# Kernel optimization log

Hardware: AMD Instinct MI355X
Metric: run time of the kernel (lower is better)

## Reference

```python
import jax, jax.numpy as jnp
import numpy as np

DIM = 16
FDIM = 16
KNN = 10
N = 1_000_000


def setup_inputs() -> dict:
    key = jax.random.key(0)
    k1, k2, k3, k4, k5, k6 = jax.random.split(key, 6)
    xknn = jax.random.normal(k1, (N, DIM, KNN), dtype=jnp.float32)
    x = jax.random.normal(k2, (N, DIM), dtype=jnp.float32)
    # mlpF = Conv1d(dim, F, 1): weight [F, dim] (kernel size 1 squeezed), bias [F]
    s = 1.0 / np.sqrt(DIM)
    Wf = jax.random.normal(k3, (FDIM, DIM), dtype=jnp.float32) * s
    bf = jax.random.normal(k4, (FDIM,), dtype=jnp.float32) * s
    # mlp1 = Conv1d(F, 1, 1): weight [F], bias scalar
    s1 = 1.0 / np.sqrt(FDIM)
    W1 = jax.random.normal(k5, (FDIM,), dtype=jnp.float32) * s1
    b1 = jax.random.normal(k6, (), dtype=jnp.float32) * s1
    return {"xknn": xknn, "x": x, "Wf": Wf, "bf": bf, "W1": W1, "b1": b1}


def reference(xknn, x, Wf, bf, W1, b1):
    n = xknn.shape[0]
    x2 = xknn.reshape(n, DIM, KNN)                       # [N, dim, K]
    # mlpF on neighbors: Conv1d(dim->F, k=1)
    h2 = jnp.einsum('fd,ndk->nfk', Wf, x2) + bf[:, None]  # [N, F, K]
    a2 = jnp.einsum('f,nfk->nk', W1, h2)[:, None, :] + b1  # mlp1 -> [N, 1, K]
    # mlpF + mlp1 on center point
    x1 = x.reshape(n, DIM, 1)
    h1 = jnp.einsum('fd,ndk->nfk', Wf, x1) + bf[:, None]   # [N, F, 1]
    a1 = jnp.einsum('f,nfk->nk', W1, h1) + b1              # [N, 1] (squeeze+unsqueeze)
    # per-slice additive attention logits (the python loop in the original)
    logits = a2 + a1[:, :, None]                           # [N, 1, K]
    # torch Fn.softmax with implicit dim on 3D tensor -> dim=0 (faithful)
    xc = jax.nn.softmax(logits, axis=0)                    # [N, 1, K]
    # values: mlpF(x2) again, then a raw reshape [N,F,K]->[N,K,F] (not transpose)
    x2v = h2.reshape(n, KNN, FDIM)                         # [N, K, F]
    x_attn = jnp.matmul(xc, x2v)                           # [N, 1, F]
    return x_attn.squeeze(), x2v
```

## Files before the change

kernel.cpp:

```cpp
#include <hip/hip_runtime.h>
#include <math.h>


__device__ __forceinline__ void comb(float& m, float& s, float om, float os) {
  float M = fmaxf(m, om);
  if (M == -INFINITY) return;
  s = s * __expf(m - M) + os * __expf(om - M);
  m = M;
}

template <int CTRL>
__device__ __forceinline__ float qb(float v) {
  return __int_as_float(__builtin_amdgcn_update_dpp(
      0, __float_as_int(v), CTRL, 0xf, 0xf, true));
}

__global__ __launch_bounds__(256) void gap_k1(
    const float* __restrict__ xknn, const float* __restrict__ x,
    const float* __restrict__ Wf, const float* __restrict__ bf,
    const float* __restrict__ W1, const float* __restrict__ b1p,
    float* __restrict__ out, float* __restrict__ partials, int n) {
  __shared__ float s_red[4][16][2];

  const int tid = threadIdx.x;
  const int q = tid & 3;
  const int lane = tid & 63;
  const int wave = tid >> 6;

  float wfq[4][16], w1q[4], bfq[4];
#pragma unroll
  for (int fp = 0; fp < 4; ++fp) {
    const float* wr = Wf + (size_t)(4 * q + fp) * 16;
#pragma unroll
    for (int dq = 0; dq < 4; ++dq) {
      float4 v = *(const float4*)(wr + dq * 4);
      wfq[fp][dq * 4 + 0] = v.x;
      wfq[fp][dq * 4 + 1] = v.y;
      wfq[fp][dq * 4 + 2] = v.z;
      wfq[fp][dq * 4 + 3] = v.w;
    }
    w1q[fp] = W1[4 * q + fp];
    bfq[fp] = bf[4 * q + fp];
  }
  const float b1v = b1p[0];

  float rm[4] = {-INFINITY, -INFINITY, -INFINITY, -INFINITY};
  float rs[4] = {0.f, 0.f, 0.f, 0.f};

  float* out0 = out;
  float* out1 = out + (size_t)n * 16;

  const long quad0 = (long)blockIdx.x * 64 + (tid >> 2);
  const long qstride = (long)gridDim.x * 64;

  for (long pt = quad0; pt < n; pt += qstride) {
    const float* rowq = xknn + (size_t)pt * 160 + 40 * q;
    float4 own[10];
#pragma unroll
    for (int j = 0; j < 10; ++j) own[j] = *(const float4*)(rowq + 4 * j);

    float acc[4][10];
#pragma unroll
    for (int fp = 0; fp < 4; ++fp)
#pragma unroll
      for (int k = 0; k < 10; ++k) acc[fp][k] = bfq[fp];

#pragma unroll
    for (int src = 0; src < 4; ++src) {
#pragma unroll
      for (int rr = 0; rr < 40; ++rr) {
        const int r = src * 40 + rr;
        const int j = rr / 4, e = rr % 4;
        const int d = r / 10, k = r - d * 10;
        const float xe = (e == 0) ? own[j].x
                       : (e == 1) ? own[j].y
                       : (e == 2) ? own[j].z
                                  : own[j].w;
        const float xv = (src == 0)   ? qb<0x00>(xe)
                         : (src == 1) ? qb<0x55>(xe)
                         : (src == 2) ? qb<0xAA>(xe)
                                      : qb<0xFF>(xe);
        acc[0][k] = fmaf(wfq[0][d], xv, acc[0][k]);
        acc[1][k] = fmaf(wfq[1][d], xv, acc[1][k]);
        acc[2][k] = fmaf(wfq[2][d], xv, acc[2][k]);
        acc[3][k] = fmaf(wfq[3][d], xv, acc[3][k]);
      }
    }

    float pa[10];
#pragma unroll
    for (int k = 0; k < 10; ++k) {
      float t = w1q[0] * acc[0][k];
      t = fmaf(w1q[1], acc[1][k], t);
      t = fmaf(w1q[2], acc[2][k], t);
      t = fmaf(w1q[3], acc[3][k], t);
      pa[k] = t;
    }
#pragma unroll
    for (int k = 0; k < 10; ++k) pa[k] += __shfl_xor(pa[k], 1);
#pragma unroll
    for (int k = 0; k < 10; ++k) pa[k] += __shfl_xor(pa[k], 2);

    const float* xr = x + (size_t)pt * 16;
    float h1[4];
#pragma unroll
    for (int fp = 0; fp < 4; ++fp) h1[fp] = bfq[fp];
#pragma unroll
    for (int dq = 0; dq < 4; ++dq) {
      float4 v = *(const float4*)(xr + dq * 4);
      float ve[4] = {v.x, v.y, v.z, v.w};
#pragma unroll
      for (int e = 0; e < 4; ++e)
#pragma unroll
        for (int fp = 0; fp < 4; ++fp)
          h1[fp] = fmaf(wfq[fp][dq * 4 + e], ve[e], h1[fp]);
    }
    float a1p = w1q[0] * h1[0];
    a1p = fmaf(w1q[1], h1[1], a1p);
    a1p = fmaf(w1q[2], h1[2], a1p);
    a1p = fmaf(w1q[3], h1[3], a1p);
    a1p += __shfl_xor(a1p, 1);
    a1p += __shfl_xor(a1p, 2);

    const float addc = a1p + 2.0f * b1v;

    float lj[4];
#pragma unroll
    for (int j = 0; j < 4; ++j) {
      const int k = 4 * q + j;
      float v = 0.f;
#pragma unroll
      for (int kk = 0; kk < 10; ++kk) v = (kk == k) ? (pa[kk] + addc) : v;
      lj[j] = v;
      if (k < 10) comb(rm[j], rs[j], v, 1.0f);
    }
    *(float4*)(out0 + (size_t)pt * 16 + 4 * q) =
        make_float4(lj[0], lj[1], lj[2], lj[3]);

    float vals[40];
#pragma unroll
    for (int fp = 0; fp < 4; ++fp)
#pragma unroll
      for (int k = 0; k < 10; ++k) vals[fp * 10 + k] = acc[fp][k];
    float* o1 = out1 + (size_t)pt * 160 + 40 * q;
#pragma unroll
    for (int i = 0; i < 10; ++i)
      *(float4*)(o1 + 4 * i) = make_float4(vals[4 * i + 0], vals[4 * i + 1],
                                           vals[4 * i + 2], vals[4 * i + 3]);
  }

#pragma unroll
  for (int mask = 4; mask < 64; mask <<= 1) {
#pragma unroll
    for (int j = 0; j < 4; ++j) {
      float om = __shfl_xor(rm[j], mask);
      float os = __shfl_xor(rs[j], mask);
      comb(rm[j], rs[j], om, os);
    }
  }
  if (lane < 4) {
#pragma unroll
    for (int j = 0; j < 4; ++j) {
      s_red[wave][lane * 4 + j][0] = rm[j];
      s_red[wave][lane * 4 + j][1] = rs[j];
    }
  }
  __syncthreads();
  if (tid < 10) {
    float m = s_red[0][tid][0], s = s_red[0][tid][1];
    comb(m, s, s_red[1][tid][0], s_red[1][tid][1]);
    comb(m, s, s_red[2][tid][0], s_red[2][tid][1]);
    comb(m, s, s_red[3][tid][0], s_red[3][tid][1]);
    partials[(size_t)blockIdx.x * 20 + tid * 2 + 0] = m;
    partials[(size_t)blockIdx.x * 20 + tid * 2 + 1] = s;
  }
}

__global__ __launch_bounds__(256) void gap_k2(const float* __restrict__ part,
                                              int nb, float* __restrict__ fin) {
  const int k = blockIdx.x;
  const int tid = threadIdx.x;
  float m = -INFINITY, s = 0.f;
  for (int i = tid; i < nb; i += 256)
    comb(m, s, part[(size_t)i * 20 + k * 2], part[(size_t)i * 20 + k * 2 + 1]);
#pragma unroll
  for (int mask = 1; mask < 64; mask <<= 1) {
    float om = __shfl_xor(m, mask, 64);
    float os = __shfl_xor(s, mask, 64);
    comb(m, s, om, os);
  }
  __shared__ float sm[4][2];
  const int wave = tid >> 6, lane = tid & 63;
  if (lane == 0) { sm[wave][0] = m; sm[wave][1] = s; }
  __syncthreads();
  if (tid == 0) {
    for (int w = 1; w < 4; ++w) comb(m, s, sm[w][0], sm[w][1]);
    fin[k * 2 + 0] = m;
    fin[k * 2 + 1] = s;
  }
}

__global__ __launch_bounds__(256) void gap_k3(const float* __restrict__ fin,
                                              float* __restrict__ out, int n) {
  __shared__ float s_fin[20];
  if (threadIdx.x < 20) s_fin[threadIdx.x] = fin[threadIdx.x];
  __syncthreads();
  float mk[10], rsk[10];
#pragma unroll
  for (int k = 0; k < 10; ++k) {
    mk[k] = s_fin[2 * k];
    rsk[k] = 1.0f / s_fin[2 * k + 1];
  }
  float* out0 = out;
  const float* out1 = out + (size_t)n * 16;
  const int q = threadIdx.x & 3;
  const int pl = threadIdx.x >> 2;
  for (long i = (long)blockIdx.x * 64 + pl; i < n; i += (long)gridDim.x * 64) {
    float* lrow = out0 + i * 16;
    float4 la = *(const float4*)(lrow);
    float4 lb = *(const float4*)(lrow + 4);
    float2 lc = *(const float2*)(lrow + 8);
    float l[10] = {la.x, la.y, la.z, la.w, lb.x, lb.y, lb.z, lb.w, lc.x, lc.y};
    float w[10];
#pragma unroll
    for (int k = 0; k < 10; ++k) w[k] = __expf(l[k] - mk[k]) * rsk[k];
    const float* vrow = out1 + i * 160 + q * 4;
    float4 acc = make_float4(0.f, 0.f, 0.f, 0.f);
#pragma unroll
    for (int k = 0; k < 10; ++k) {
      float4 v = *(const float4*)(vrow + k * 16);
      float wk = w[k];
      acc.x = fmaf(wk, v.x, acc.x);
      acc.y = fmaf(wk, v.y, acc.y);
      acc.z = fmaf(wk, v.z, acc.z);
      acc.w = fmaf(wk, v.w, acc.w);
    }
    *(float4*)(lrow + q * 4) = acc;
  }
}

extern "C" void kernel_launch(void* const* d_in, const int* in_sizes, int n_in,
                              void* d_out, int out_size, void* d_ws, size_t ws_size,
                              hipStream_t stream) {
  const float* xknn = (const float*)d_in[0];
  const float* x    = (const float*)d_in[1];
  const float* Wf   = (const float*)d_in[2];
  const float* bf   = (const float*)d_in[3];
  const float* W1   = (const float*)d_in[4];
  const float* b1   = (const float*)d_in[5];
  float* out = (float*)d_out;
  const int n = in_sizes[1] / 16;

  const int G1 = 2048;
  float* partials = (float*)d_ws;
  float* finals = partials + (size_t)G1 * 20;

  gap_k1<<<G1, 256, 0, stream>>>(xknn, x, Wf, bf, W1, b1, out, partials, n);
  gap_k2<<<10, 256, 0, stream>>>(partials, G1, finals);
  gap_k3<<<2048, 256, 0, stream>>>(finals, out, n);
}
```

Baseline: 562.0 us.

## Software-prefetch next row, fold W1 into Wf for logits, halve k1 grid

The main kernel now loads the next point's xknn and x data into registers while computing the current point, so load latency overlaps with compute. Logits are computed from a precomputed combined vector u = W1·Wf and a folded bias constant, instead of reducing the full hidden activations. This lets the logit path run independently of the DPP-broadcast matmul. The grid is halved and launch bounds request 2 blocks per CU. In exchange, the prefetch buffers raise register pressure and there is extra arithmetic for the separate logit dot products.

```diff
diff --git a/kernel.cpp b/kernel.cpp
--- a/kernel.cpp
+++ b/kernel.cpp
@@ -15,7 +15,11 @@
       0, __float_as_int(v), CTRL, 0xf, 0xf, true));
 }
 
-__global__ __launch_bounds__(256) void gap_k1(
+__device__ __forceinline__ float f4e(const float4& v, int e) {
+  return (e == 0) ? v.x : (e == 1) ? v.y : (e == 2) ? v.z : v.w;
+}
+
+__global__ __launch_bounds__(256, 2) void gap_k1(
     const float* __restrict__ xknn, const float* __restrict__ x,
     const float* __restrict__ Wf, const float* __restrict__ bf,
     const float* __restrict__ W1, const float* __restrict__ b1p,
@@ -27,7 +31,8 @@
   const int lane = tid & 63;
   const int wave = tid >> 6;
 
-  float wfq[4][16], w1q[4], bfq[4];
+  float wfq[4][16], bfq[4];
+  float w1q[4];
 #pragma unroll
   for (int fp = 0; fp < 4; ++fp) {
     const float* wr = Wf + (size_t)(4 * q + fp) * 16;
@@ -44,6 +49,36 @@
   }
   const float b1v = b1p[0];
 
+  float ufull[16];
+#pragma unroll
+  for (int d = 0; d < 16; ++d) {
+    float t = w1q[0] * wfq[0][d];
+    t = fmaf(w1q[1], wfq[1][d], t);
+    t = fmaf(w1q[2], wfq[2][d], t);
+    t = fmaf(w1q[3], wfq[3][d], t);
+    ufull[d] = t;
+  }
+#pragma unroll
+  for (int d = 0; d < 16; ++d) ufull[d] += __shfl_xor(ufull[d], 1);
+#pragma unroll
+  for (int d = 0; d < 16; ++d) ufull[d] += __shfl_xor(ufull[d], 2);
+  float u4[4];
+#pragma unroll
+  for (int i = 0; i < 4; ++i) {
+    float v = ufull[i];
+    v = (q == 1) ? ufull[4 + i] : v;
+    v = (q == 2) ? ufull[8 + i] : v;
+    v = (q == 3) ? ufull[12 + i] : v;
+    u4[i] = v;
+  }
+  float sb = w1q[0] * bfq[0];
+  sb = fmaf(w1q[1], bfq[1], sb);
+  sb = fmaf(w1q[2], bfq[2], sb);
+  sb = fmaf(w1q[3], bfq[3], sb);
+  sb += __shfl_xor(sb, 1);
+  sb += __shfl_xor(sb, 2);
+  const float addK = 2.0f * (sb + b1v);
+
   float rm[4] = {-INFINITY, -INFINITY, -INFINITY, -INFINITY};
   float rs[4] = {0.f, 0.f, 0.f, 0.f};
 
@@ -53,29 +88,58 @@
   const long quad0 = (long)blockIdx.x * 64 + (tid >> 2);
   const long qstride = (long)gridDim.x * 64;
 
+  float4 cur[10], xc;
+  {
+    const long p0 = (quad0 < n) ? quad0 : 0;
+    const float* rowq = xknn + (size_t)p0 * 160 + 40 * q;
+#pragma unroll
+    for (int j = 0; j < 10; ++j) cur[j] = *(const float4*)(rowq + 4 * j);
+    xc = *(const float4*)(x + (size_t)p0 * 16 + 4 * q);
+  }
+
   for (long pt = quad0; pt < n; pt += qstride) {
-    const float* rowq = xknn + (size_t)pt * 160 + 40 * q;
-    float4 own[10];
-#pragma unroll
-    for (int j = 0; j < 10; ++j) own[j] = *(const float4*)(rowq + 4 * j);
+    const long ptn = pt + qstride;
+    const long ptl = (ptn < n) ? ptn : pt;
+    float4 nxt[10], xn;
+    {
+      const float* rowq = xknn + (size_t)ptl * 160 + 40 * q;
+#pragma unroll
+      for (int j = 0; j < 10; ++j) nxt[j] = *(const float4*)(rowq + 4 * j);
+      xn = *(const float4*)(x + (size_t)ptl * 16 + 4 * q);
+    }
+
+    float pa[10];
+#pragma unroll
+    for (int k = 0; k < 10; ++k) pa[k] = 0.f;
+#pragma unroll
+    for (int rr = 0; rr < 40; ++rr) {
+      const int dl = rr / 10, k = rr - dl * 10;
+      pa[k] = fmaf(u4[dl], f4e(cur[rr / 4], rr % 4), pa[k]);
+    }
+    float a1u = u4[0] * xc.x;
+    a1u = fmaf(u4[1], xc.y, a1u);
+    a1u = fmaf(u4[2], xc.z, a1u);
+    a1u = fmaf(u4[3], xc.w, a1u);
+#pragma unroll
+    for (int k = 0; k < 10; ++k) pa[k] += __shfl_xor(pa[k], 1);
+#pragma unroll
+    for (int k = 0; k < 10; ++k) pa[k] += __shfl_xor(pa[k], 2);
+    a1u += __shfl_xor(a1u, 1);
+    a1u += __shfl_xor(a1u, 2);
+    const float addc = a1u + addK;
 
     float acc[4][10];
 #pragma unroll
     for (int fp = 0; fp < 4; ++fp)
 #pragma unroll
       for (int k = 0; k < 10; ++k) acc[fp][k] = bfq[fp];
-
 #pragma unroll
     for (int src = 0; src < 4; ++src) {
 #pragma unroll
       for (int rr = 0; rr < 40; ++rr) {
         const int r = src * 40 + rr;
-        const int j = rr / 4, e = rr % 4;
         const int d = r / 10, k = r - d * 10;
-        const float xe = (e == 0) ? own[j].x
-                       : (e == 1) ? own[j].y
-                       : (e == 2) ? own[j].z
-                                  : own[j].w;
+        const float xe = f4e(cur[rr / 4], rr % 4);
         const float xv = (src == 0)   ? qb<0x00>(xe)
                          : (src == 1) ? qb<0x55>(xe)
                          : (src == 2) ? qb<0xAA>(xe)
@@ -87,43 +151,6 @@
       }
     }
 
-    float pa[10];
-#pragma unroll
-    for (int k = 0; k < 10; ++k) {
-      float t = w1q[0] * acc[0][k];
-      t = fmaf(w1q[1], acc[1][k], t);
-      t = fmaf(w1q[2], acc[2][k], t);
-      t = fmaf(w1q[3], acc[3][k], t);
-      pa[k] = t;
-    }
-#pragma unroll
-    for (int k = 0; k < 10; ++k) pa[k] += __shfl_xor(pa[k], 1);
-#pragma unroll
-    for (int k = 0; k < 10; ++k) pa[k] += __shfl_xor(pa[k], 2);
-
-    const float* xr = x + (size_t)pt * 16;
-    float h1[4];
-#pragma unroll
-    for (int fp = 0; fp < 4; ++fp) h1[fp] = bfq[fp];
-#pragma unroll
-    for (int dq = 0; dq < 4; ++dq) {
-      float4 v = *(const float4*)(xr + dq * 4);
-      float ve[4] = {v.x, v.y, v.z, v.w};
-#pragma unroll
-      for (int e = 0; e < 4; ++e)
-#pragma unroll
-        for (int fp = 0; fp < 4; ++fp)
-          h1[fp] = fmaf(wfq[fp][dq * 4 + e], ve[e], h1[fp]);
-    }
-    float a1p = w1q[0] * h1[0];
-    a1p = fmaf(w1q[1], h1[1], a1p);
-    a1p = fmaf(w1q[2], h1[2], a1p);
-    a1p = fmaf(w1q[3], h1[3], a1p);
-    a1p += __shfl_xor(a1p, 1);
-    a1p += __shfl_xor(a1p, 2);
-
-    const float addc = a1p + 2.0f * b1v;
-
     float lj[4];
 #pragma unroll
     for (int j = 0; j < 4; ++j) {
@@ -137,16 +164,18 @@
     *(float4*)(out0 + (size_t)pt * 16 + 4 * q) =
         make_float4(lj[0], lj[1], lj[2], lj[3]);
 
-    float vals[40];
-#pragma unroll
-    for (int fp = 0; fp < 4; ++fp)
-#pragma unroll
-      for (int k = 0; k < 10; ++k) vals[fp * 10 + k] = acc[fp][k];
     float* o1 = out1 + (size_t)pt * 160 + 40 * q;
 #pragma unroll
-    for (int i = 0; i < 10; ++i)
-      *(float4*)(o1 + 4 * i) = make_float4(vals[4 * i + 0], vals[4 * i + 1],
-                                           vals[4 * i + 2], vals[4 * i + 3]);
+    for (int i = 0; i < 10; ++i) {
+      const int j0 = 4 * i, j1 = 4 * i + 1, j2 = 4 * i + 2, j3 = 4 * i + 3;
+      *(float4*)(o1 + 4 * i) =
+          make_float4(acc[j0 / 10][j0 % 10], acc[j1 / 10][j1 % 10],
+                      acc[j2 / 10][j2 % 10], acc[j3 / 10][j3 % 10]);
+    }
+
+#pragma unroll
+    for (int j = 0; j < 10; ++j) cur[j] = nxt[j];
+    xc = xn;
   }
 
 #pragma unroll
@@ -251,7 +280,7 @@
   float* out = (float*)d_out;
   const int n = in_sizes[1] / 16;
 
-  const int G1 = 2048;
+  const int G1 = 1024;
   float* partials = (float*)d_ws;
   float* finals = partials + (size_t)G1 * 20;
 
```

Result: slower. 1.302 ms (+131.7%).

## Fold mlp1 into mlpF weights for logits, stage Wf in LDS, halve grid

Applied to the files above, without the earlier changes.

Precomputes u = W1·Wf and the folded bias so the attention logits come from a 16-wide dot product on the raw inputs, not a reduction over the 16 features. Wf is staged transposed in shared memory and read as float4 per d instead of being held as 64 registers per thread, which lowers register pressure (launch bounds now request 2 blocks). The k1 grid is halved to 1024 blocks. The change trades per-thread register weights for LDS reads and slightly alters the floating-point summation order.

```diff
diff --git a/kernel.cpp b/kernel.cpp
--- a/kernel.cpp
+++ b/kernel.cpp
@@ -15,11 +15,17 @@
       0, __float_as_int(v), CTRL, 0xf, 0xf, true));
 }
 
-__global__ __launch_bounds__(256) void gap_k1(
+__device__ __forceinline__ float f4e(const float4& v, int e) {
+  return (e == 0) ? v.x : (e == 1) ? v.y : (e == 2) ? v.z : v.w;
+}
+
+__global__ __launch_bounds__(256, 2) void gap_k1(
     const float* __restrict__ xknn, const float* __restrict__ x,
     const float* __restrict__ Wf, const float* __restrict__ bf,
     const float* __restrict__ W1, const float* __restrict__ b1p,
     float* __restrict__ out, float* __restrict__ partials, int n) {
+  __shared__ float s_wfT[16][16];
+  __shared__ float s_w1[16];
   __shared__ float s_red[4][16][2];
 
   const int tid = threadIdx.x;
@@ -27,22 +33,26 @@
   const int lane = tid & 63;
   const int wave = tid >> 6;
 
-  float wfq[4][16], w1q[4], bfq[4];
-#pragma unroll
-  for (int fp = 0; fp < 4; ++fp) {
-    const float* wr = Wf + (size_t)(4 * q + fp) * 16;
-#pragma unroll
-    for (int dq = 0; dq < 4; ++dq) {
-      float4 v = *(const float4*)(wr + dq * 4);
-      wfq[fp][dq * 4 + 0] = v.x;
-      wfq[fp][dq * 4 + 1] = v.y;
-      wfq[fp][dq * 4 + 2] = v.z;
-      wfq[fp][dq * 4 + 3] = v.w;
-    }
-    w1q[fp] = W1[4 * q + fp];
-    bfq[fp] = bf[4 * q + fp];
-  }
-  const float b1v = b1p[0];
+  {
+    const int f = tid & 15, d = tid >> 4;
+    if (tid < 256) s_wfT[d][f] = Wf[f * 16 + d];
+    if (tid < 16) s_w1[tid] = W1[tid];
+  }
+  __syncthreads();
+
+  float u4[4];
+#pragma unroll
+  for (int dd = 0; dd < 4; ++dd) {
+    float t = 0.f;
+#pragma unroll
+    for (int f = 0; f < 16; ++f) t = fmaf(s_w1[f], s_wfT[4 * q + dd][f], t);
+    u4[dd] = t;
+  }
+  float sb = 0.f;
+#pragma unroll
+  for (int f = 0; f < 16; ++f) sb = fmaf(s_w1[f], bf[f], sb);
+  const float addA = sb + 2.0f * b1p[0];
+  const float4 bfq = *(const float4*)(bf + 4 * q);
 
   float rm[4] = {-INFINITY, -INFINITY, -INFINITY, -INFINITY};
   float rs[4] = {0.f, 0.f, 0.f, 0.f};
@@ -50,79 +60,62 @@
   float* out0 = out;
   float* out1 = out + (size_t)n * 16;
 
-  const long quad0 = (long)blockIdx.x * 64 + (tid >> 2);
-  const long qstride = (long)gridDim.x * 64;
-
-  for (long pt = quad0; pt < n; pt += qstride) {
+  const long pt0 = (long)blockIdx.x * 64 + (tid >> 2);
+  const long pstride = (long)gridDim.x * 64;
+
+  for (long pt = pt0; pt < n; pt += pstride) {
     const float* rowq = xknn + (size_t)pt * 160 + 40 * q;
     float4 own[10];
 #pragma unroll
     for (int j = 0; j < 10; ++j) own[j] = *(const float4*)(rowq + 4 * j);
-
-    float acc[4][10];
-#pragma unroll
-    for (int fp = 0; fp < 4; ++fp)
-#pragma unroll
-      for (int k = 0; k < 10; ++k) acc[fp][k] = bfq[fp];
-
-#pragma unroll
-    for (int src = 0; src < 4; ++src) {
-#pragma unroll
-      for (int rr = 0; rr < 40; ++rr) {
-        const int r = src * 40 + rr;
-        const int j = rr / 4, e = rr % 4;
-        const int d = r / 10, k = r - d * 10;
-        const float xe = (e == 0) ? own[j].x
-                       : (e == 1) ? own[j].y
-                       : (e == 2) ? own[j].z
-                                  : own[j].w;
-        const float xv = (src == 0)   ? qb<0x00>(xe)
-                         : (src == 1) ? qb<0x55>(xe)
-                         : (src == 2) ? qb<0xAA>(xe)
-                                      : qb<0xFF>(xe);
-        acc[0][k] = fmaf(wfq[0][d], xv, acc[0][k]);
-        acc[1][k] = fmaf(wfq[1][d], xv, acc[1][k]);
-        acc[2][k] = fmaf(wfq[2][d], xv, acc[2][k]);
-        acc[3][k] = fmaf(wfq[3][d], xv, acc[3][k]);
+    const float4 xc4 = *(const float4*)(x + (size_t)pt * 16 + 4 * q);
+
+    float pa[10];
+#pragma unroll
+    for (int k = 0; k < 10; ++k) pa[k] = 0.f;
+#pragma unroll
+    for (int rr = 0; rr < 40; ++rr) {
+      const int dl = rr / 10, k = rr - dl * 10;
+      pa[k] = fmaf(u4[dl], f4e(own[rr >> 2], rr & 3), pa[k]);
+    }
+#pragma unroll
+    for (int k = 0; k < 10; ++k) pa[k] += __shfl_xor(pa[k], 1);
+#pragma unroll
+    for (int k = 0; k < 10; ++k) pa[k] += __shfl_xor(pa[k], 2);
+    float a1u = u4[0] * xc4.x;
+    a1u = fmaf(u4[1], xc4.y, a1u);
+    a1u = fmaf(u4[2], xc4.z, a1u);
+    a1u = fmaf(u4[3], xc4.w, a1u);
+    a1u += __shfl_xor(a1u, 1);
+    a1u += __shfl_xor(a1u, 2);
+    const float addc = a1u + addA;
+
+    float acc0[10], acc1[10], acc2[10], acc3[10];
+#pragma unroll
+    for (int k = 0; k < 10; ++k) {
+      acc0[k] = bfq.x;
+      acc1[k] = bfq.y;
+      acc2[k] = bfq.z;
+      acc3[k] = bfq.w;
+    }
+#pragma unroll
+    for (int d = 0; d < 16; ++d) {
+      const float4 wfv = *(const float4*)(&s_wfT[d][4 * q]);
+      const int dd = d & 3;
+#pragma unroll
+      for (int j = 0; j < 10; ++j) {
+        const int e = 10 * dd + j;
+        const float mine = f4e(own[e >> 2], e & 3);
+        const float xv = ((d >> 2) == 0)   ? qb<0x00>(mine)
+                         : ((d >> 2) == 1) ? qb<0x55>(mine)
+                         : ((d >> 2) == 2) ? qb<0xAA>(mine)
+                                           : qb<0xFF>(mine);
+        acc0[j] = fmaf(wfv.x, xv, acc0[j]);
+        acc1[j] = fmaf(wfv.y, xv, acc1[j]);
+        acc2[j] = fmaf(wfv.z, xv, acc2[j]);
+        acc3[j] = fmaf(wfv.w, xv, acc3[j]);
       }
     }
-
-    float pa[10];
-#pragma unroll
-    for (int k = 0; k < 10; ++k) {
-      float t = w1q[0] * acc[0][k];
-      t = fmaf(w1q[1], acc[1][k], t);
-      t = fmaf(w1q[2], acc[2][k], t);
-      t = fmaf(w1q[3], acc[3][k], t);
-      pa[k] = t;
-    }
-#pragma unroll
-    for (int k = 0; k < 10; ++k) pa[k] += __shfl_xor(pa[k], 1);
-#pragma unroll
-    for (int k = 0; k < 10; ++k) pa[k] += __shfl_xor(pa[k], 2);
-
-    const float* xr = x + (size_t)pt * 16;
-    float h1[4];
-#pragma unroll
-    for (int fp = 0; fp < 4; ++fp) h1[fp] = bfq[fp];
-#pragma unroll
-    for (int dq = 0; dq < 4; ++dq) {
-      float4 v = *(const float4*)(xr + dq * 4);
-      float ve[4] = {v.x, v.y, v.z, v.w};
-#pragma unroll
-      for (int e = 0; e < 4; ++e)
-#pragma unroll
-        for (int fp = 0; fp < 4; ++fp)
-          h1[fp] = fmaf(wfq[fp][dq * 4 + e], ve[e], h1[fp]);
-    }
-    float a1p = w1q[0] * h1[0];
-    a1p = fmaf(w1q[1], h1[1], a1p);
-    a1p = fmaf(w1q[2], h1[2], a1p);
-    a1p = fmaf(w1q[3], h1[3], a1p);
-    a1p += __shfl_xor(a1p, 1);
-    a1p += __shfl_xor(a1p, 2);
-
-    const float addc = a1p + 2.0f * b1v;
 
     float lj[4];
 #pragma unroll
@@ -137,16 +130,17 @@
     *(float4*)(out0 + (size_t)pt * 16 + 4 * q) =
         make_float4(lj[0], lj[1], lj[2], lj[3]);
 
-    float vals[40];
-#pragma unroll
-    for (int fp = 0; fp < 4; ++fp)
-#pragma unroll
-      for (int k = 0; k < 10; ++k) vals[fp * 10 + k] = acc[fp][k];
     float* o1 = out1 + (size_t)pt * 160 + 40 * q;
-#pragma unroll
-    for (int i = 0; i < 10; ++i)
-      *(float4*)(o1 + 4 * i) = make_float4(vals[4 * i + 0], vals[4 * i + 1],
-                                           vals[4 * i + 2], vals[4 * i + 3]);
+    *(float4*)(o1 + 0) = make_float4(acc0[0], acc0[1], acc0[2], acc0[3]);
+    *(float4*)(o1 + 4) = make_float4(acc0[4], acc0[5], acc0[6], acc0[7]);
+    *(float4*)(o1 + 8) = make_float4(acc0[8], acc0[9], acc1[0], acc1[1]);
+    *(float4*)(o1 + 12) = make_float4(acc1[2], acc1[3], acc1[4], acc1[5]);
+    *(float4*)(o1 + 16) = make_float4(acc1[6], acc1[7], acc1[8], acc1[9]);
+    *(float4*)(o1 + 20) = make_float4(acc2[0], acc2[1], acc2[2], acc2[3]);
+    *(float4*)(o1 + 24) = make_float4(acc2[4], acc2[5], acc2[6], acc2[7]);
+    *(float4*)(o1 + 28) = make_float4(acc2[8], acc2[9], acc3[0], acc3[1]);
+    *(float4*)(o1 + 32) = make_float4(acc3[2], acc3[3], acc3[4], acc3[5]);
+    *(float4*)(o1 + 36) = make_float4(acc3[6], acc3[7], acc3[8], acc3[9]);
   }
 
 #pragma unroll
@@ -251,7 +245,7 @@
   float* out = (float*)d_out;
   const int n = in_sizes[1] / 16;
 
-  const int G1 = 2048;
+  const int G1 = 1024;
   float* partials = (float*)d_ws;
   float* finals = partials + (size_t)G1 * 20;
 
```

Measured after the change: 925.4 us. 1.65x slower.
